# Performance work log

Measured on AMD Instinct MI355X. Metric: run time of the kernel, lower is better.

The kernel has to match this reference:

```python
import math
import jax, jax.numpy as jnp
import numpy as np

EMBED_DIM = 1024
NUM_HEADS = 16
SEGMENT_LENGTHS = [1024, 1024, 2048, 4096]
DILATION_RATES = [1, 2, 4, 8]
BATCH = 2
SEQ_LEN = 8192


def _xy2d(n, x, y):
    # Vectorized Hilbert curve xy -> d for an n x n grid (n power of 2).
    x = x.astype(np.int64).copy()
    y = y.astype(np.int64).copy()
    d = np.zeros_like(x)
    s = n // 2
    while s > 0:
        rx = ((x & s) > 0).astype(np.int64)
        ry = ((y & s) > 0).astype(np.int64)
        d += s * s * ((3 * rx) ^ ry)
        swap = ry == 0
        flip = swap & (rx == 1)
        x = np.where(flip, s - 1 - x, x)
        y = np.where(flip, s - 1 - y, y)
        xs = np.where(swap, y, x)
        ys = np.where(swap, x, y)
        x, y = xs, ys
        s //= 2
    return d


def _hilbert_perm(L):
    # Returns (perm, inv): new[i] = old[perm[i]] (Hilbert order), inv undoes it.
    if L <= 1:
        p = np.arange(L, dtype=np.int64)
        return p, p
    side = 1 << int(math.ceil(math.log2(L) / 2.0))  # side^2 >= L
    idx = np.arange(side * side, dtype=np.int64)
    xg = idx % side
    yg = idx // side
    d = _xy2d(side, xg, yg)
    order = np.argsort(d, kind='stable')  # linear cell indices in Hilbert order
    perm = order[order < L]
    inv = np.empty(L, dtype=np.int64)
    inv[perm] = np.arange(L, dtype=np.int64)
    return perm, inv


def _dilated_attention(q, k, v, rate, scale):
    # q,k,v: [B,H,L,D]; attention within residue-class groups (positions i with i % rate == j).
    B, H, L, D = q.shape
    if rate > 1:
        g = L // rate
        q = q.reshape(B, H, g, rate, D).transpose(0, 1, 3, 2, 4)  # [B,H,r,g,D]
        k = k.reshape(B, H, g, rate, D).transpose(0, 1, 3, 2, 4)
        v = v.reshape(B, H, g, rate, D).transpose(0, 1, 3, 2, 4)
    scores = jnp.einsum('...qd,...kd->...qk', q, k) * scale
    attn = jax.nn.softmax(scores, axis=-1)
    out = jnp.einsum('...qk,...kd->...qd', attn, v)
    if rate > 1:
        out = out.transpose(0, 1, 3, 2, 4).reshape(B, H, L, D)
    return out


def _forward(x, w_qkv, b_qkv, w_out, b_out):
    B, S, E = x.shape
    H = NUM_HEADS
    Dh = E // H
    scale = 1.0 / math.sqrt(Dh)
    qkv = x @ w_qkv.T + b_qkv                       # [B,S,3E]
    qkv = qkv.reshape(B, S, 3, H, Dh).transpose(2, 0, 3, 1, 4)  # [3,B,H,S,Dh]
    q, k, v = qkv[0], qkv[1], qkv[2]
    outs = []
    pos = 0
    for seg_len, rate in zip(SEGMENT_LENGTHS, DILATION_RATES):
        if pos >= S:
            break
        end = min(pos + seg_len, S)
        L = end - pos
        qs = q[:, :, pos:end]
        ks = k[:, :, pos:end]
        vs = v[:, :, pos:end]
        if L > 1:
            perm_np, inv_np = _hilbert_perm(L)
            perm = jnp.asarray(perm_np)
            inv = jnp.asarray(inv_np)
            qs = qs[:, :, perm]
            ks = ks[:, :, perm]
            vs = vs[:, :, perm]
        seg_out = _dilated_attention(qs, ks, vs, rate, scale)
        if L > 1:
            seg_out = seg_out[:, :, inv]
        outs.append(seg_out)
        pos = end
    out = jnp.concatenate(outs, axis=2)             # [B,H,S,Dh]
    out = out.transpose(0, 2, 1, 3).reshape(B, S, E)
    return out @ w_out.T + b_out


def setup_inputs() -> dict:
    key = jax.random.key(0)
    k1, k2, k3 = jax.random.split(key, 3)
    E = EMBED_DIM
    return {
        'x': jax.random.normal(k1, (BATCH, SEQ_LEN, E), dtype=jnp.float32),
        'w_qkv': jax.random.normal(k2, (3 * E, E), dtype=jnp.float32) * 0.02,
        'b_qkv': jnp.zeros((3 * E,), dtype=jnp.float32),
        'w_out': jax.random.normal(k3, (E, E), dtype=jnp.float32) * 0.02,
        'b_out': jnp.zeros((E,), dtype=jnp.float32),
    }


def reference(x, w_qkv, b_qkv, w_out, b_out):
    return _forward(x, w_qkv, b_qkv, w_out, b_out)
```

## Files before the change

kernel.cpp:

```cpp
#include <hip/hip_runtime.h>
#include <hip/hip_bf16.h>
#include <math.h>

#define S_LEN 8192
#define NH 16
#define DH 64
#define BB 2
#define EE 1024

typedef float floatx4 __attribute__((ext_vector_type(4)));
typedef float f32x4 __attribute__((ext_vector_type(4)));
typedef short bf16x8 __attribute__((ext_vector_type(8)));
typedef _Float16 f16x8 __attribute__((ext_vector_type(8)));
typedef int i32x4 __attribute__((ext_vector_type(4)));
typedef unsigned short u16x4 __attribute__((ext_vector_type(4)));

__device__ inline unsigned short f2bf(float x) {
  unsigned int u = __builtin_bit_cast(unsigned int, x);
  u += 0x7FFFu + ((u >> 16) & 1u);
  return (unsigned short)(u >> 16);
}

__device__ inline void async_copy16(void* lds, const void* g) {
  __builtin_amdgcn_global_load_lds(
      (const __attribute__((address_space(1))) void*)g,
      (__attribute__((address_space(3))) void*)lds, 16, 0, 0);
}

__device__ inline int hilbert_xy2d(int n, int x, int y) {
  int d = 0;
  for (int s = n >> 1; s > 0; s >>= 1) {
    int rx = (x & s) ? 1 : 0;
    int ry = (y & s) ? 1 : 0;
    d += s * s * ((3 * rx) ^ ry);
    if (ry == 0) {
      if (rx == 1) { x = s - 1 - x; y = s - 1 - y; }
      int t = x; x = y; y = t;
    }
  }
  return d;
}

__global__ void build_idx_kernel(int* __restrict__ idx) {
  __shared__ int order[4096];
  __shared__ int perm[4096];
  __shared__ int cnts[256];
  const int seg = blockIdx.x;
  const int posA[4] = {0, 1024, 2048, 4096};
  const int LA[4]   = {1024, 1024, 2048, 4096};
  const int pos = posA[seg];
  const int L = LA[seg];
  const int lr = seg;
  const int side  = (L <= 1024) ? 32 : 64;
  const int lside = (L <= 1024) ? 5 : 6;
  const int cells = side * side;
  const int tid = threadIdx.x;

  for (int c = tid; c < cells; c += 256) {
    int x = c & (side - 1);
    int y = c >> lside;
    order[hilbert_xy2d(side, x, y)] = c;
  }
  __syncthreads();

  if (L == cells) {
    for (int t = tid; t < L; t += 256) perm[t] = order[t];
  } else {
    const int per = cells >> 8;
    const int base = tid * per;
    int cnt = 0;
    for (int u = 0; u < per; ++u) cnt += (order[base + u] < L) ? 1 : 0;
    cnts[tid] = cnt;
    __syncthreads();
    if (tid == 0) {
      int s = 0;
      for (int i = 0; i < 256; ++i) { int c0 = cnts[i]; cnts[i] = s; s += c0; }
    }
    __syncthreads();
    int r = cnts[tid];
    for (int u = 0; u < per; ++u) {
      int o = order[base + u];
      if (o < L) perm[r++] = o;
    }
  }
  __syncthreads();

  const int g = L >> lr;
  const int rm = (1 << lr) - 1;
  for (int t = tid; t < L; t += 256) {
    int j = t & rm;
    int i = t >> lr;
    idx[pos + j * g + i] = pos + perm[t];
  }
}

__global__ __launch_bounds__(256) void tof16_kernel(
    const float* __restrict__ in, unsigned short* __restrict__ hi, int n) {
  int base = (blockIdx.x * 256 + threadIdx.x) * 8;
  if (base >= n) return;
  floatx4 v0 = *(const floatx4*)(in + base);
  floatx4 v1 = *(const floatx4*)(in + base + 4);
  u16x4 h0, h1;
#pragma unroll
  for (int i = 0; i < 4; ++i) {
    h0[i] = __builtin_bit_cast(unsigned short, (_Float16)v0[i]);
    h1[i] = __builtin_bit_cast(unsigned short, (_Float16)v1[i]);
  }
  *(u16x4*)(hi + base) = h0;
  *(u16x4*)(hi + base + 4) = h1;
}

template<int MODE>
__global__ __launch_bounds__(256, 2) void mgemm_kernel(
    const unsigned short* __restrict__ Ah, const unsigned short* __restrict__ Bh,
    const float* __restrict__ bias, float* __restrict__ Cf,
    unsigned short* __restrict__ q_h, unsigned short* __restrict__ k_h,
    unsigned short* __restrict__ v_h,
    int N, int K) {
  __shared__ short lds[3][12288];
  const int tid = threadIdx.x;
  const int lane = tid & 63;
  const int w = tid >> 6;
  const int wr = w >> 1, wc = w & 1;
  const int bm0 = blockIdx.x * 128;
  const int bn0 = blockIdx.y * 256;

  const unsigned short* sp[6];
  int dofs[6];
#pragma unroll
  for (int ii = 0; ii < 6; ++ii) {
    int e = w * 6 + ii;
    const unsigned short* base = (e < 8) ? Ah : Bh;
    int row0 = (e < 8) ? (bm0 + e * 16) : (bn0 + (e - 8) * 16);
    int dof = (e < 8) ? (e * 512) : (4096 + (e - 8) * 512);
    sp[ii] = base + (size_t)(row0 + (lane & 15)) * K + (lane >> 4) * 8;
    dofs[ii] = dof;
  }

  f32x4 acc[4][8];
#pragma unroll
  for (int m = 0; m < 4; ++m)
#pragma unroll
    for (int n = 0; n < 8; ++n) acc[m][n] = (f32x4)0.f;

  const int nk = K >> 5;
#pragma unroll
  for (int ii = 0; ii < 6; ++ii) async_copy16(&lds[0][dofs[ii]], sp[ii]);
#pragma unroll
  for (int ii = 0; ii < 6; ++ii) async_copy16(&lds[1][dofs[ii]], sp[ii] + 32);
  asm volatile("s_waitcnt vmcnt(6)" ::: "memory");
  __builtin_amdgcn_s_barrier();

  for (int t = 0; t < nk; ++t) {
    const short* lb = &lds[0][0] + (t % 3) * 12288;

    if (t + 2 < nk) {
      short* db = &lds[0][0] + ((t + 2) % 3) * 12288;
      const int k0 = (t + 2) * 32;
#pragma unroll
      for (int ii = 0; ii < 6; ++ii) async_copy16(db + dofs[ii], sp[ii] + k0);
    }

    f16x8 ah[4], bf[8];
#pragma unroll
    for (int m = 0; m < 4; ++m)
      ah[m] = *(const f16x8*)&lb[(wr * 4 + m) * 512 + lane * 8];
#pragma unroll
    for (int n = 0; n < 8; ++n)
      bf[n] = *(const f16x8*)&lb[4096 + (wc * 8 + n) * 512 + lane * 8];

    __builtin_amdgcn_s_setprio(1);
#pragma unroll
    for (int m = 0; m < 4; ++m)
#pragma unroll
      for (int n = 0; n < 8; ++n)
        acc[m][n] = __builtin_amdgcn_mfma_f32_16x16x32_f16(ah[m], bf[n], acc[m][n], 0, 0, 0);
    __builtin_amdgcn_s_setprio(0);

    if (t + 2 < nk) {
      asm volatile("s_waitcnt vmcnt(6)" ::: "memory");
    } else {
      asm volatile("s_waitcnt vmcnt(0)" ::: "memory");
    }
    if (t + 1 < nk) __builtin_amdgcn_s_barrier();
  }

  const int rq = lane >> 4;
  const int cl = lane & 15;
#pragma unroll
  for (int n = 0; n < 8; ++n) {
    const int gn = bn0 + wc * 128 + n * 16 + cl;
    const float bv = bias[gn];
    if (MODE == 0) {
      const int which = gn >> 10;
      const int hh = (gn >> 6) & 15;
      const int d = gn & 63;
      unsigned short* dsth = (which == 0) ? q_h : (which == 1) ? k_h : v_h;
#pragma unroll
      for (int m = 0; m < 4; ++m)
#pragma unroll
        for (int j = 0; j < 4; ++j) {
          const int gm = bm0 + wr * 64 + m * 16 + rq * 4 + j;
          const int b = gm >> 13;
          const int s = gm & 8191;
          float val = acc[m][n][j] + bv;
          size_t off = ((size_t)(b * NH + hh) * S_LEN + s) * DH + d;
          if (which == 2) {
            dsth[off] = __builtin_bit_cast(unsigned short, (_Float16)val);
          } else {
            float sc = (which == 0) ? 0.18033688f : 1.0f;
            dsth[off] = f2bf(val * sc);
          }
        }
    } else {
#pragma unroll
      for (int m = 0; m < 4; ++m)
#pragma unroll
        for (int j = 0; j < 4; ++j) {
          const int gm = bm0 + wr * 64 + m * 16 + rq * 4 + j;
          Cf[(size_t)gm * N + gn] = acc[m][n][j] + bv;
        }
    }
  }
}

__global__ __launch_bounds__(256, 2) void mattn_kernel(
    const unsigned short* __restrict__ qh, const unsigned short* __restrict__ kh,
    const unsigned short* __restrict__ vh, const int* __restrict__ idx,
    unsigned short* __restrict__ oh) {
  __shared__ __align__(16) char smem[53248];
  int* idxg = (int*)(smem + 49152);

  const int tid = threadIdx.x;
  const int lane = tid & 63;
  const int w = tid >> 6;
  const int g = lane >> 4;
  const int q = lane & 15;

  const int c = blockIdx.x;
  const int bh = blockIdx.y;
  const int bb = bh >> 4;
  const int h = bh & 15;
  int gbase, glen, q0;
  if (c < 4) { gbase = 0; glen = 1024; q0 = c * 256; }
  else { int t = c - 4; gbase = 1024 + (t >> 1) * 512; glen = 512; q0 = (t & 1) * 256; }

  for (int i = tid; i < glen; i += 256) idxg[i] = idx[gbase + i];
  __syncthreads();

  const size_t bhoff = (size_t)(bb * NH + h) * S_LEN * DH;
  const unsigned short* qhb = qh + bhoff;
  const unsigned short* khb = kh + bhoff;
  const unsigned short* vhb = vh + bhoff;

  int qrow[4];
#pragma unroll
  for (int qt = 0; qt < 4; ++qt) qrow[qt] = idxg[q0 + w * 64 + qt * 16 + q];

  f32x4 oacc[4][4];
#pragma unroll
  for (int dt = 0; dt < 4; ++dt)
#pragma unroll
    for (int qt = 0; qt < 4; ++qt) oacc[dt][qt] = (f32x4)0.f;
  float lq[4] = {0.f, 0.f, 0.f, 0.f};

  const int p = tid & 31;
  const int dg = tid >> 5;
  char* vb = smem + 32768;

  bf16x8 VA, VB;

#pragma unroll
  for (int ii = 0; ii < 2; ++ii) {
    int g8 = w * 2 + ii;
    int r = g8 * 8 + (lane >> 3);
    int bsw = (lane & 7) ^ (r & 7);
    async_copy16(smem + g8 * 1024, khb + (size_t)idxg[r] * DH + bsw * 8);
  }
  {
    int r0 = idxg[2 * p], r1 = idxg[2 * p + 1];
    VA = *(const bf16x8*)(vhb + (size_t)r0 * DH + dg * 8);
    VB = *(const bf16x8*)(vhb + (size_t)r1 * DH + dg * 8);
  }

  const int nt = glen >> 6;
  for (int kt_ = 0; kt_ < nt; ++kt_) {
    const int kt0 = kt_ * 64;
    const char* kb = smem + (kt_ & 1) * 16384;

    asm volatile("s_waitcnt vmcnt(0)" ::: "memory");
    __builtin_amdgcn_s_barrier();

#pragma unroll
    for (int u = 0; u < 8; ++u) {
      unsigned int w32 = (unsigned int)(unsigned short)VA[u] |
                         ((unsigned int)(unsigned short)VB[u] << 16);
      int d = dg * 8 + u;
      int byte_ = (d * 128 + p * 4) ^ ((d & 7) << 4);
      *(unsigned int*)(vb + byte_) = w32;
    }

    if (kt_ + 1 < nt) {
      char* kbn = smem + ((kt_ + 1) & 1) * 16384;
#pragma unroll
      for (int ii = 0; ii < 2; ++ii) {
        int g8 = w * 2 + ii;
        int r = g8 * 8 + (lane >> 3);
        int bsw = (lane & 7) ^ (r & 7);
        async_copy16(kbn + g8 * 1024,
                     khb + (size_t)idxg[kt0 + 64 + r] * DH + bsw * 8);
      }
      int r0 = idxg[kt0 + 64 + 2 * p], r1 = idxg[kt0 + 64 + 2 * p + 1];
      VA = *(const bf16x8*)(vhb + (size_t)r0 * DH + dg * 8);
      VB = *(const bf16x8*)(vhb + (size_t)r1 * DH + dg * 8);
    }

    asm volatile("s_waitcnt lgkmcnt(0)" ::: "memory");
    __builtin_amdgcn_s_barrier();

    f32x4 sacc[4][4];
#pragma unroll
    for (int qt = 0; qt < 4; ++qt)
#pragma unroll
      for (int kt = 0; kt < 4; ++kt) sacc[qt][kt] = (f32x4)0.f;
#pragma unroll
    for (int dc = 0; dc < 2; ++dc) {
      bf16x8 kf[4];
#pragma unroll
      for (int kt = 0; kt < 4; ++kt) {
        int r = q + 16 * kt;
        int byte_ = (r * 128 + g * 16 + dc * 64) ^ ((r & 7) << 4);
        kf[kt] = *(const bf16x8*)(kb + byte_);
      }
#pragma unroll
      for (int qt = 0; qt < 4; ++qt) {
        bf16x8 qhf = *(const bf16x8*)(qhb + (size_t)qrow[qt] * DH + dc * 32 + g * 8);
#pragma unroll
        for (int kt = 0; kt < 4; ++kt)
          sacc[qt][kt] = __builtin_amdgcn_mfma_f32_16x16x32_bf16(kf[kt], qhf, sacc[qt][kt], 0, 0, 0);
      }
    }

    i32x4 pfh[4][2];
#pragma unroll
    for (int qt = 0; qt < 4; ++qt) {
      float su = 0.f;
#pragma unroll
      for (int kt = 0; kt < 4; ++kt)
#pragma unroll
        for (int j = 0; j < 4; ++j) {
          float pv = __builtin_amdgcn_exp2f(sacc[qt][kt][j] - 4.0f);
          sacc[qt][kt][j] = pv;
          su += pv;
        }
      su += __shfl_xor(su, 16);
      su += __shfl_xor(su, 32);
      lq[qt] += su;
      unsigned int eh[4][2];
#pragma unroll
      for (int kt = 0; kt < 4; ++kt)
#pragma unroll
        for (int pp = 0; pp < 2; ++pp) {
          unsigned int ba =
              (unsigned int)__builtin_bit_cast(unsigned short, (_Float16)sacc[qt][kt][2 * pp]);
          unsigned int bb2 =
              (unsigned int)__builtin_bit_cast(unsigned short, (_Float16)sacc[qt][kt][2 * pp + 1]);
          eh[kt][pp] = ba | (bb2 << 16);
        }
#pragma unroll
      for (int kc = 0; kc < 2; ++kc) {
        i32x4 fh;
#pragma unroll
        for (int t = 0; t < 4; ++t) {
          int src = q + 32 * (g & 1) + 16 * (t >> 1);
          int ah = __shfl((int)eh[2 * kc][t & 1], src);
          int bh2 = __shfl((int)eh[2 * kc + 1][t & 1], src);
          fh[t] = (g >> 1) ? bh2 : ah;
        }
        pfh[qt][kc] = fh;
      }
    }

#pragma unroll
    for (int kc = 0; kc < 2; ++kc)
#pragma unroll
      for (int dt = 0; dt < 4; ++dt) {
        int r = q + 16 * dt;
        int byte_ = (r * 128 + g * 16 + kc * 64) ^ ((r & 7) << 4);
        f16x8 vf = *(const f16x8*)(vb + byte_);
#pragma unroll
        for (int qt = 0; qt < 4; ++qt) {
          f16x8 ph = __builtin_bit_cast(f16x8, pfh[qt][kc]);
          oacc[dt][qt] = __builtin_amdgcn_mfma_f32_16x16x32_f16(vf, ph, oacc[dt][qt], 0, 0, 0);
        }
      }
  }

#pragma unroll
  for (int qt = 0; qt < 4; ++qt) {
    float inv = 1.f / lq[qt];
    size_t obase = ((size_t)bb * S_LEN + qrow[qt]) * EE + h * DH;
#pragma unroll
    for (int dt = 0; dt < 4; ++dt) {
      u16x4 hv;
#pragma unroll
      for (int j = 0; j < 4; ++j)
        hv[j] = __builtin_bit_cast(unsigned short, (_Float16)(oacc[dt][qt][j] * inv));
      *(u16x4*)(oh + obase + dt * 16 + g * 4) = hv;
    }
  }
}

extern "C" void kernel_launch(void* const* d_in, const int* in_sizes, int n_in,
                              void* d_out, int out_size, void* d_ws, size_t ws_size,
                              hipStream_t stream) {
  const float* x     = (const float*)d_in[0];
  const float* w_qkv = (const float*)d_in[1];
  const float* b_qkv = (const float*)d_in[2];
  const float* w_out = (const float*)d_in[3];
  const float* b_out = (const float*)d_in[4];
  float* outp = (float*)d_out;

  const size_t per = (size_t)BB * S_LEN * EE;
  const size_t nwq = (size_t)3 * EE * EE;
  const size_t nwo = (size_t)EE * EE;

  unsigned short* khb = (unsigned short*)d_ws;
  unsigned short* vhb = khb + per;
  unsigned short* xh  = vhb + per;
  unsigned short* wqh = xh + per;
  unsigned short* woh = wqh + nwq;
  int* idx = (int*)(woh + nwo);

  unsigned short* qhb = (unsigned short*)d_out;
  unsigned short* ah  = xh;

  build_idx_kernel<<<4, 256, 0, stream>>>(idx);
  tof16_kernel<<<(int)(per / 2048), 256, 0, stream>>>(x, xh, (int)per);
  tof16_kernel<<<(int)(nwq / 2048), 256, 0, stream>>>(w_qkv, wqh, (int)nwq);
  tof16_kernel<<<(int)(nwo / 2048), 256, 0, stream>>>(w_out, woh, (int)nwo);

  mgemm_kernel<0><<<dim3(128, 12), 256, 0, stream>>>(
      xh, wqh, b_qkv, nullptr, qhb, khb, vhb, 3 * EE, EE);
  mattn_kernel<<<dim3(32, 32), 256, 0, stream>>>(qhb, khb, vhb, idx, ah);
  mgemm_kernel<1><<<dim3(128, 4), 256, 0, stream>>>(
      ah, woh, b_out, outp, nullptr, nullptr, nullptr, EE, EE);
}
```

Measured before the change: 375.0 us.

## Double attention block to 512 threads to share K/V tiles across more queries

```diff
diff --git a/kernel.cpp b/kernel.cpp
--- a/kernel.cpp
+++ b/kernel.cpp
@@ -224,16 +224,18 @@
   }
 }
 
-__global__ __launch_bounds__(256, 2) void mattn_kernel(
+__global__ __launch_bounds__(512, 2) void mattn_kernel(
     const unsigned short* __restrict__ qh, const unsigned short* __restrict__ kh,
     const unsigned short* __restrict__ vh, const int* __restrict__ idx,
     unsigned short* __restrict__ oh) {
-  __shared__ __align__(16) char smem[53248];
-  int* idxg = (int*)(smem + 49152);
+  __shared__ __align__(16) char smem[28672];
+  int* idxg = (int*)(smem + 24576);
 
   const int tid = threadIdx.x;
   const int lane = tid & 63;
   const int w = tid >> 6;
+  const int wg = w >> 2;
+  const int w4 = w & 3;
   const int g = lane >> 4;
   const int q = lane & 15;
 
@@ -241,11 +243,11 @@
   const int bh = blockIdx.y;
   const int bb = bh >> 4;
   const int h = bh & 15;
-  int gbase, glen, q0;
-  if (c < 4) { gbase = 0; glen = 1024; q0 = c * 256; }
-  else { int t = c - 4; gbase = 1024 + (t >> 1) * 512; glen = 512; q0 = (t & 1) * 256; }
-
-  for (int i = tid; i < glen; i += 256) idxg[i] = idx[gbase + i];
+  int gbase, glen, cb;
+  if (c < 2) { gbase = 0; glen = 1024; cb = c * 512; }
+  else { gbase = 1024 + (c - 2) * 512; glen = 512; cb = 0; }
+
+  for (int i = tid; i < glen; i += 512) idxg[i] = idx[gbase + i];
   __syncthreads();
 
   const size_t bhoff = (size_t)(bb * NH + h) * S_LEN * DH;
@@ -253,9 +255,10 @@
   const unsigned short* khb = kh + bhoff;
   const unsigned short* vhb = vh + bhoff;
 
+  const int q0 = cb + wg * 256 + w4 * 64;
   int qrow[4];
 #pragma unroll
-  for (int qt = 0; qt < 4; ++qt) qrow[qt] = idxg[q0 + w * 64 + qt * 16 + q];
+  for (int qt = 0; qt < 4; ++qt) qrow[qt] = idxg[q0 + qt * 16 + q];
 
   f32x4 oacc[4][4];
 #pragma unroll
@@ -265,19 +268,17 @@
   float lq[4] = {0.f, 0.f, 0.f, 0.f};
 
   const int p = tid & 31;
-  const int dg = tid >> 5;
-  char* vb = smem + 32768;
+  const int dg = (tid >> 5) & 7;
+  char* vb = smem + 16384;
 
   bf16x8 VA, VB;
 
-#pragma unroll
-  for (int ii = 0; ii < 2; ++ii) {
-    int g8 = w * 2 + ii;
-    int r = g8 * 8 + (lane >> 3);
+  {
+    int r = w * 8 + (lane >> 3);
     int bsw = (lane & 7) ^ (r & 7);
-    async_copy16(smem + g8 * 1024, khb + (size_t)idxg[r] * DH + bsw * 8);
-  }
-  {
+    async_copy16(smem + w * 1024, khb + (size_t)idxg[r] * DH + bsw * 8);
+  }
+  if (tid < 256) {
     int r0 = idxg[2 * p], r1 = idxg[2 * p + 1];
     VA = *(const bf16x8*)(vhb + (size_t)r0 * DH + dg * 8);
     VB = *(const bf16x8*)(vhb + (size_t)r1 * DH + dg * 8);
@@ -286,33 +287,35 @@
   const int nt = glen >> 6;
   for (int kt_ = 0; kt_ < nt; ++kt_) {
     const int kt0 = kt_ * 64;
-    const char* kb = smem + (kt_ & 1) * 16384;
+    const char* kb = smem + (kt_ & 1) * 8192;
 
     asm volatile("s_waitcnt vmcnt(0)" ::: "memory");
     __builtin_amdgcn_s_barrier();
 
-#pragma unroll
-    for (int u = 0; u < 8; ++u) {
-      unsigned int w32 = (unsigned int)(unsigned short)VA[u] |
-                         ((unsigned int)(unsigned short)VB[u] << 16);
-      int d = dg * 8 + u;
-      int byte_ = (d * 128 + p * 4) ^ ((d & 7) << 4);
-      *(unsigned int*)(vb + byte_) = w32;
+    if (tid < 256) {
+#pragma unroll
+      for (int u = 0; u < 8; ++u) {
+        unsigned int w32 = (unsigned int)(unsigned short)VA[u] |
+                           ((unsigned int)(unsigned short)VB[u] << 16);
+        int d = dg * 8 + u;
+        int byte_ = (d * 128 + p * 4) ^ ((d & 7) << 4);
+        *(unsigned int*)(vb + byte_) = w32;
+      }
     }
 
     if (kt_ + 1 < nt) {
-      char* kbn = smem + ((kt_ + 1) & 1) * 16384;
-#pragma unroll
-      for (int ii = 0; ii < 2; ++ii) {
-        int g8 = w * 2 + ii;
-        int r = g8 * 8 + (lane >> 3);
+      char* kbn = smem + ((kt_ + 1) & 1) * 8192;
+      {
+        int r = w * 8 + (lane >> 3);
         int bsw = (lane & 7) ^ (r & 7);
-        async_copy16(kbn + g8 * 1024,
+        async_copy16(kbn + w * 1024,
                      khb + (size_t)idxg[kt0 + 64 + r] * DH + bsw * 8);
       }
-      int r0 = idxg[kt0 + 64 + 2 * p], r1 = idxg[kt0 + 64 + 2 * p + 1];
-      VA = *(const bf16x8*)(vhb + (size_t)r0 * DH + dg * 8);
-      VB = *(const bf16x8*)(vhb + (size_t)r1 * DH + dg * 8);
+      if (tid < 256) {
+        int r0 = idxg[kt0 + 64 + 2 * p], r1 = idxg[kt0 + 64 + 2 * p + 1];
+        VA = *(const bf16x8*)(vhb + (size_t)r0 * DH + dg * 8);
+        VB = *(const bf16x8*)(vhb + (size_t)r1 * DH + dg * 8);
+      }
     }
 
     asm volatile("s_waitcnt lgkmcnt(0)" ::: "memory");
@@ -442,7 +445,7 @@
 
   mgemm_kernel<0><<<dim3(128, 12), 256, 0, stream>>>(
       xh, wqh, b_qkv, nullptr, qhb, khb, vhb, 3 * EE, EE);
-  mattn_kernel<<<dim3(32, 32), 256, 0, stream>>>(qhb, khb, vhb, idx, ah);
+  mattn_kernel<<<dim3(16, 32), 512, 0, stream>>>(qhb, khb, vhb, idx, ah);
   mgemm_kernel<1><<<dim3(128, 4), 256, 0, stream>>>(
       ah, woh, b_out, outp, nullptr, nullptr, nullptr, EE, EE);
 }
```

Measured after the change: 410.3 us. 9.4% more time.
